# Optimization experiments

Hardware: AMD Instinct MI355X
Metric: run time of the kernel (lower is better)

## Reference

```python
import jax, jax.numpy as jnp
import numpy as np

B, SQ, SKV, E, H = 4, 2048, 2048, 1024, 16
HD = E // H  # 64


def stablemax(x):
    # StableMax: s(x) = x+1 if x>=0 else 1/(1-x), normalized along last axis
    s = jnp.where(x >= 0, x + 1.0, 1.0 / (1.0 - x))
    return s / jnp.sum(s, axis=-1, keepdims=True)


def setup_inputs() -> dict:
    key = jax.random.key(0)
    ks = jax.random.split(key, 6)
    scale = 1.0 / np.sqrt(E)
    return {
        "query": jax.random.normal(ks[0], (B, SQ, E), jnp.float32),
        "key_value": jax.random.normal(ks[1], (B, SKV, E), jnp.float32),
        "Wq": jax.random.normal(ks[2], (E, E), jnp.float32) * scale,
        "bq": jnp.zeros((E,), jnp.float32),
        "Wk": jax.random.normal(ks[3], (E, E), jnp.float32) * scale,
        "bk": jnp.zeros((E,), jnp.float32),
        "Wv": jax.random.normal(ks[4], (E, E), jnp.float32) * scale,
        "bv": jnp.zeros((E,), jnp.float32),
        "Wo": jax.random.normal(ks[5], (E, E), jnp.float32) * scale,
        "bo": jnp.zeros((E,), jnp.float32),
    }


def reference(query, key_value, Wq, bq, Wk, bk, Wv, bv, Wo, bo):
    b = query.shape[0]
    # linear projections (torch Linear: x @ W^T + b)
    q = query @ Wq.T + bq
    k = key_value @ Wk.T + bk
    v = key_value @ Wv.T + bv
    # [B, H, S, HD]
    q = q.reshape(b, -1, H, HD).transpose(0, 2, 1, 3)
    k = k.reshape(b, -1, H, HD).transpose(0, 2, 1, 3)
    v = v.reshape(b, -1, H, HD).transpose(0, 2, 1, 3)
    scores = jnp.einsum("bhqd,bhkd->bhqk", q, k) / np.sqrt(HD).astype(np.float32)
    attn = stablemax(scores)  # dropout is identity in eval mode
    context = jnp.einsum("bhqk,bhkd->bhqd", attn, v)
    context = context.transpose(0, 2, 1, 3).reshape(b, -1, E)
    return context @ Wo.T + bo
```

## Files before the change

### kernel.cpp

```cpp
#include <hip/hip_runtime.h>

typedef __bf16 bf16;
typedef __bf16 bf16x8 __attribute__((ext_vector_type(8)));
typedef __bf16 bf16x4 __attribute__((ext_vector_type(4)));
typedef _Float16 f16;
typedef _Float16 f16x2 __attribute__((ext_vector_type(2)));
typedef _Float16 f16x4 __attribute__((ext_vector_type(4)));
typedef _Float16 f16x8 __attribute__((ext_vector_type(8)));
typedef __fp16 h16x2 __attribute__((ext_vector_type(2)));
typedef float f32x4 __attribute__((ext_vector_type(4)));

__device__ __forceinline__ f32x4 mfma_qk(bf16x8 a, bf16x8 b, f32x4 c) {
    return __builtin_amdgcn_mfma_f32_16x16x32_bf16(a, b, c, 0, 0, 0);
}
__device__ __forceinline__ f32x4 mfma_pv32(f16x8 a, f16x8 b, f32x4 c) {
    return __builtin_amdgcn_mfma_f32_16x16x32_f16(a, b, c, 0, 0, 0);
}
__device__ __forceinline__ f16x2 pkrtz(float a, float b) {
    h16x2 r = __builtin_amdgcn_cvt_pkrtz(a, b);
    return __builtin_bit_cast(f16x2, r);
}

#define GLOAD_LDS16(gp, lp)                                                    \
    __builtin_amdgcn_global_load_lds(                                          \
        (const __attribute__((address_space(1))) unsigned int*)(gp),           \
        (__attribute__((address_space(3))) unsigned int*)(lp), 16, 0, 0)

#define PWAIT4 asm volatile("s_waitcnt vmcnt(4) lgkmcnt(0)\ns_barrier" ::: "memory")
#define PWAIT2 asm volatile("s_waitcnt vmcnt(2) lgkmcnt(0)\ns_barrier" ::: "memory")
#define PWAIT0 asm volatile("s_waitcnt vmcnt(0) lgkmcnt(0)\ns_barrier" ::: "memory")

__global__ __launch_bounds__(256) void cast_inputs(
    const float* __restrict__ w0, const float* __restrict__ w1,
    const float* __restrict__ w2, const float* __restrict__ w3,
    const float* __restrict__ kv, const float* __restrict__ q,
    bf16* __restrict__ Wb, bf16* __restrict__ KVa, bf16* __restrict__ Qb) {
    long i4 = (long)blockIdx.x * 256 + threadIdx.x;
    const float* src;
    bf16* dst;
    long loc;
    float sc = 1.0f;
    if (i4 < 1048576) {
        int which = (int)(i4 >> 18);
        loc = (i4 & 262143) << 2;
        src = which == 0 ? w0 : which == 1 ? w1 : which == 2 ? w2 : w3;
        dst = Wb + ((long)which << 20);
        if (which == 0) sc = 0.125f;
    } else if (i4 < 3145728) {
        loc = (i4 - 1048576) << 2;
        src = kv; dst = KVa;
    } else {
        loc = (i4 - 3145728) << 2;
        src = q; dst = Qb;
    }
    float4 f = *(const float4*)(src + loc);
    bf16x4 o;
    o[0] = (bf16)(f.x * sc); o[1] = (bf16)(f.y * sc);
    o[2] = (bf16)(f.z * sc); o[3] = (bf16)(f.w * sc);
    *(bf16x4*)(dst + loc) = o;
}

__device__ __forceinline__ void gemm_core(
    const bf16* __restrict__ A, const bf16* __restrict__ Wt,
    const float* __restrict__ bias, void* __restrict__ Yv,
    const int om, bf16* smem, const int n0, const int m0, const float bsc) {
    constexpr int Kd = 1024, Nd = 1024;
    constexpr int TP = 132;
    char* sbytes = (char*)smem;
    const int tid = threadIdx.x;
    const int wid = tid >> 6, lane = tid & 63;
    const int l16 = lane & 15, quad = lane >> 4;
    const int mh = (wid >> 1) * 64, nh = (wid & 1) * 64;

    const int rS = tid >> 2;
    const int cS = (tid & 3) ^ (rS & 3);
    const bf16* Asrc = A + (long)(m0 + rS) * Kd + cS * 8;
    const bf16* Bsrc = Wt + (long)(n0 + rS) * Kd + cS * 8;

    const int aOff = (mh + l16) * 64 + ((quad ^ (l16 & 3)) << 4);
    const int bOff = 8192 + (nh + l16) * 64 + ((quad ^ (l16 & 3)) << 4);

    f32x4 acc[4][4];
#pragma unroll
    for (int i = 0; i < 4; ++i)
#pragma unroll
        for (int j = 0; j < 4; ++j) acc[i][j] = (f32x4){0.f, 0.f, 0.f, 0.f};

    auto stageK = [&](int step, int b) {
        const int kt = step * 32;
        char* base = sbytes + b * 16384;
        GLOAD_LDS16(Asrc + kt, base + tid * 16);
        GLOAD_LDS16(Asrc + 64 * Kd + kt, base + 4096 + tid * 16);
        GLOAD_LDS16(Bsrc + kt, base + 8192 + tid * 16);
        GLOAD_LDS16(Bsrc + 64 * Kd + kt, base + 12288 + tid * 16);
    };

    auto computeK = [&](int b) {
        const char* base = sbytes + b * 16384;
        bf16x8 af[4], bq[4];
#pragma unroll
        for (int i = 0; i < 4; ++i) af[i] = *(const bf16x8*)(base + aOff + i * 1024);
#pragma unroll
        for (int i = 0; i < 4; ++i) bq[i] = *(const bf16x8*)(base + bOff + i * 1024);
#pragma unroll
        for (int i = 0; i < 4; ++i)
#pragma unroll
            for (int j = 0; j < 4; ++j)
                acc[i][j] = mfma_qk(af[i], bq[j], acc[i][j]);
    };

    stageK(0, 0);
    stageK(1, 1);
#pragma unroll 1
    for (int t = 0; t < 30; t += 3) {
        PWAIT4; stageK(t + 2, 2); computeK(0);
        PWAIT4; stageK(t + 3, 0); computeK(1);
        PWAIT4; stageK(t + 4, 1); computeK(2);
    }
    PWAIT4; computeK(0);
    PWAIT0; computeK(1);
    __syncthreads();

    if (om == 2) {
#pragma unroll
        for (int j = 0; j < 4; ++j) {
            const int col = nh + j * 16 + l16;
            const float bv = bias[n0 + col] * bsc;
#pragma unroll
            for (int i = 0; i < 4; ++i)
#pragma unroll
                for (int p = 0; p < 2; ++p) {
                    f16x2 pk2;
                    pk2[0] = (f16)(acc[i][j][p * 2 + 0] + bv);
                    pk2[1] = (f16)(acc[i][j][p * 2 + 1] + bv);
                    *(f16x2*)&smem[col * TP + mh + i * 16 + quad * 4 + p * 2] = pk2;
                }
        }
        __syncthreads();
        const int b_ = m0 >> 11, skv0 = m0 & 2047;
        const int rowc = tid & 15;
        const int B32 = (rowc >> 2) * 32, g4 = (rowc & 3) * 4;
        const f16* sm = (const f16*)smem;
#pragma unroll
        for (int c = 0; c < 8; ++c) {
            const int col = (tid >> 4) + c * 16;
            const int colg = n0 + col;
            f16x4 lo = *(const f16x4*)&sm[col * TP + B32 + g4];
            f16x4 hi = *(const f16x4*)&sm[col * TP + B32 + 16 + g4];
            f16x8 v = __builtin_shufflevector(lo, hi, 0, 1, 2, 3, 4, 5, 6, 7);
            const long base = ((long)((b_ * 16 + (colg >> 6)) * 64 + (colg & 63))) << 11;
            *(f16x8*)((f16*)Yv + base + skv0 + rowc * 8) = v;
        }
    } else {
#pragma unroll
        for (int j = 0; j < 4; ++j) {
            const int col = n0 + nh + j * 16 + l16;
            const float bv = bias[col] * bsc;
#pragma unroll
            for (int i = 0; i < 4; ++i)
#pragma unroll
                for (int r = 0; r < 4; ++r) {
                    int row = m0 + mh + i * 16 + quad * 4 + r;
                    float v = acc[i][j][r] + bv;
                    if (om == 1)
                        ((float*)Yv)[(long)row * Nd + col] = v;
                    else
                        ((bf16*)Yv)[(long)row * Nd + col] = (bf16)v;
                }
        }
    }
}

__global__ __launch_bounds__(256) void proj_qkv(
    const bf16* __restrict__ Qb, const bf16* __restrict__ KVa,
    const bf16* __restrict__ Wb,
    const float* __restrict__ bq, const float* __restrict__ bk,
    const float* __restrict__ bv,
    bf16* __restrict__ Qw, bf16* __restrict__ Kw, f16* __restrict__ Vt) {
    __shared__ __align__(16) bf16 smem[24576];
    const int lin = blockIdx.x + (blockIdx.y << 3) + (blockIdx.z << 9);
    const int nid = (lin & 7) * 192 + (lin >> 3);
    const int z = nid >> 9, rem = nid & 511;
    const int n0 = (rem & 7) << 7, m0 = (rem >> 3) << 7;
    if (z == 0)
        gemm_core(Qb, Wb, bq, Qw, 0, smem, n0, m0, 0.125f);
    else if (z == 1)
        gemm_core(KVa, Wb + (1l << 20), bk, Kw, 0, smem, n0, m0, 1.0f);
    else
        gemm_core(KVa, Wb + (2l << 20), bv, Vt, 2, smem, n0, m0, 1.0f);
}

__global__ __launch_bounds__(256) void gemm_o(
    const bf16* __restrict__ Cw, const bf16* __restrict__ Wo,
    const float* __restrict__ bo, float* __restrict__ out) {
    __shared__ __align__(16) bf16 smem[24576];
    const int lin = blockIdx.x + (blockIdx.y << 3);
    const int nid = (lin & 7) * 64 + (lin >> 3);
    gemm_core(Cw, Wo, bo, out, 1, smem, (nid & 7) << 7, (nid >> 3) << 7, 1.0f);
}

__global__ __launch_bounds__(256) void attn_kernel(
    const bf16* __restrict__ Q, const bf16* __restrict__ K,
    const f16* __restrict__ Vt, bf16* __restrict__ C) {
    constexpr int E = 1024, S = 2048;
    __shared__ __align__(16) char smem_raw[24576];

    const int tid = threadIdx.x;
    const int wid = tid >> 6, lane = tid & 63;
    const int l16 = lane & 15, quad = lane >> 4;
    const int l7 = l16 & 7, l3 = l16 & 3;
    const int lin = blockIdx.x + (blockIdx.y << 4) + (blockIdx.z << 8);
    const int nid = (lin & 7) * 128 + (lin >> 3);
    const int qt = nid & 15, h = (nid >> 4) & 15, b = nid >> 8;

    const long q0 = (long)b * S + qt * 128;
    const bf16* Qg = Q + q0 * E + h * 64;
    const bf16* Kg = K + (long)b * S * E + h * 64;
    const f16* Vg = Vt + ((long)(b * 16 + h) << 17);

    bf16x8 qf[2][2];
#pragma unroll
    for (int mt = 0; mt < 2; ++mt)
#pragma unroll
        for (int kc = 0; kc < 2; ++kc)
            qf[mt][kc] = *(const bf16x8*)(Qg + (long)(wid * 32 + mt * 16 + l16) * E + kc * 32 + quad * 8);
    asm volatile("s_waitcnt vmcnt(0)" ::: "memory");

    const bf16* Ksrc = Kg + (long)(tid >> 3) * E + (((tid & 7) ^ ((tid >> 3) & 7)) * 8);
    const f16* Vsrc = Vg + (long)(tid >> 2) * S + (((tid & 3) ^ ((tid >> 2) & 3)) * 8);

    int ka0[3], ka1[3], va[3];
#pragma unroll
    for (int i = 0; i < 3; ++i) {
        ka0[i] = i * 8192 + l16 * 128 + ((quad ^ l7) << 4);
        ka1[i] = i * 8192 + l16 * 128 + (((quad + 4) ^ l7) << 4);
        va[i]  = i * 8192 + 4096 + l16 * 64 + ((quad ^ l3) << 4);
    }

    f16x8 ones8;
#pragma unroll
    for (int j = 0; j < 8; ++j) ones8[j] = (f16)1.0f;

    f32x4 ctx[2][4];
    f32x4 dacc[2];
#pragma unroll
    for (int mt = 0; mt < 2; ++mt) {
        dacc[mt] = (f32x4){0.f, 0.f, 0.f, 0.f};
#pragma unroll
        for (int dt = 0; dt < 4; ++dt) ctx[mt][dt] = (f32x4){0.f, 0.f, 0.f, 0.f};
    }

    auto stage = [&](int kv0, int bi) {
        GLOAD_LDS16(Ksrc + (long)kv0 * E, smem_raw + bi * 8192 + tid * 16);
        GLOAD_LDS16(Vsrc + kv0, smem_raw + bi * 8192 + 4096 + tid * 16);
    };

    auto compute = [&](int bi) {
        f32x4 sacc[2][2];
#pragma unroll
        for (int sh = 0; sh < 2; ++sh) {
            bf16x8 kf0 = *(const bf16x8*)(smem_raw + ka0[bi] + sh * 2048);
            bf16x8 kf1 = *(const bf16x8*)(smem_raw + ka1[bi] + sh * 2048);
            __builtin_amdgcn_s_setprio(1);
#pragma unroll
            for (int mt = 0; mt < 2; ++mt) {
                f32x4 t = mfma_qk(kf0, qf[mt][0], (f32x4){0.f, 0.f, 0.f, 0.f});
                sacc[sh][mt] = mfma_qk(kf1, qf[mt][1], t);
            }
            __builtin_amdgcn_s_setprio(0);
        }
        f16x8 pp[2];
#pragma unroll
        for (int mt = 0; mt < 2; ++mt) {
            float sv[8];
#pragma unroll
            for (int sh = 0; sh < 2; ++sh)
#pragma unroll
                for (int r = 0; r < 4; ++r) {
                    float x = sacc[sh][mt][r];
                    float u = __builtin_fabsf(x) + 1.0f;
                    sv[sh * 4 + r] = (x >= 0.f) ? u : __builtin_amdgcn_rcpf(u);
                }
            f16x2 w0 = pkrtz(sv[0], sv[1]);
            f16x2 w1 = pkrtz(sv[2], sv[3]);
            f16x2 w2 = pkrtz(sv[4], sv[5]);
            f16x2 w3 = pkrtz(sv[6], sv[7]);
            f16x4 lo = __builtin_shufflevector(w0, w1, 0, 1, 2, 3);
            f16x4 hi = __builtin_shufflevector(w2, w3, 0, 1, 2, 3);
            pp[mt] = __builtin_shufflevector(lo, hi, 0, 1, 2, 3, 4, 5, 6, 7);
        }
        __builtin_amdgcn_s_setprio(1);
        dacc[0] = mfma_pv32(ones8, pp[0], dacc[0]);
        dacc[1] = mfma_pv32(ones8, pp[1], dacc[1]);
        __builtin_amdgcn_s_setprio(0);
#pragma unroll
        for (int dt = 0; dt < 4; ++dt) {
            f16x8 vf = *(const f16x8*)(smem_raw + va[bi] + dt * 1024);
            __builtin_amdgcn_s_setprio(1);
#pragma unroll
            for (int mt = 0; mt < 2; ++mt)
                ctx[mt][dt] = mfma_pv32(vf, pp[mt], ctx[mt][dt]);
            __builtin_amdgcn_s_setprio(0);
        }
    };

    stage(0, 0);
    stage(32, 1);
    int kv = 64;
#pragma unroll 1
    for (int it = 0; it < 20; ++it) {
        PWAIT2; stage(kv, 2); compute(0); kv += 32;
        PWAIT2; stage(kv, 0); compute(1); kv += 32;
        PWAIT2; stage(kv, 1); compute(2); kv += 32;
    }
    PWAIT2; stage(kv, 2); compute(0);
    PWAIT2; stage(kv + 32, 0); compute(1);
    PWAIT2; compute(2);
    PWAIT0; compute(0);
    __syncthreads();

    float scl[2];
#pragma unroll
    for (int mt = 0; mt < 2; ++mt) scl[mt] = __builtin_amdgcn_rcpf(dacc[mt][0]);

    bf16* Os = (bf16*)smem_raw;
#pragma unroll
    for (int mt = 0; mt < 2; ++mt)
#pragma unroll
        for (int dt = 0; dt < 4; ++dt) {
            bf16x4 o;
#pragma unroll
            for (int r = 0; r < 4; ++r) o[r] = (bf16)(ctx[mt][dt][r] * scl[mt]);
            *(bf16x4*)&Os[(wid * 32 + mt * 16 + l16) * 68 + dt * 16 + quad * 4] = o;
        }
    __syncthreads();
    {
        const int r = tid >> 1, c = (tid & 1) * 32;
        bf16* cp = C + (q0 + r) * E + h * 64 + c;
#pragma unroll
        for (int j = 0; j < 4; ++j)
            *(bf16x8*)(cp + j * 8) = *(const bf16x8*)&Os[r * 68 + c + j * 8];
    }
}

extern "C" void kernel_launch(void* const* d_in, const int* in_sizes, int n_in,
                              void* d_out, int out_size, void* d_ws, size_t ws_size,
                              hipStream_t stream) {
    const float* query = (const float*)d_in[0];
    const float* keyv  = (const float*)d_in[1];
    const float* Wq = (const float*)d_in[2];
    const float* bq = (const float*)d_in[3];
    const float* Wk = (const float*)d_in[4];
    const float* bk = (const float*)d_in[5];
    const float* Wv = (const float*)d_in[6];
    const float* bv = (const float*)d_in[7];
    const float* Wo = (const float*)d_in[8];
    const float* bo = (const float*)d_in[9];

    char* ws = (char*)d_ws;
    bf16* Wb  = (bf16*)ws;
    bf16* KVa = (bf16*)(ws + (8l << 20));
    bf16* Qb  = (bf16*)(ws + (24l << 20));
    bf16* Qw  = (bf16*)(ws + (40l << 20));
    f16*  Vt  = (f16*)(ws + (56l << 20));
    bf16* Kw  = (bf16*)d_out;
    bf16* Cw  = KVa;

    cast_inputs<<<20480, 256, 0, stream>>>(Wq, Wk, Wv, Wo, keyv, query, Wb, KVa, Qb);

    proj_qkv<<<dim3(8, 64, 3), 256, 0, stream>>>(Qb, KVa, Wb, bq, bk, bv, Qw, Kw, Vt);

    attn_kernel<<<dim3(16, 16, 4), 256, 0, stream>>>(Qw, Kw, Vt, Cw);

    gemm_o<<<dim3(8, 64), 256, 0, stream>>>(Cw, Wb + (3l << 20), bo, (float*)d_out);
}
```

Before: 309.6 us.

## Rewrite output GEMM with 128x64 tiles and triple-buffered pipeline; grid-stride cast

Replaces the shared gemm_core call for the output projection with a dedicated kernel using 128x64 tiles, a K step of 32 and a three-stage global-to-LDS ring buffer with vmcnt(3) waits. The grid doubles to 1024 blocks, which should fill the GPU's compute units better for the 8192x1024 output GEMM. The cast kernel becomes a grid-stride loop over a quarter as many blocks, so each thread converts several elements. Smaller tiles lower per-block reuse and add more A-tile reloads.

```diff
diff --git a/kernel.cpp b/kernel.cpp
--- a/kernel.cpp
+++ b/kernel.cpp
@@ -27,6 +27,7 @@
         (__attribute__((address_space(3))) unsigned int*)(lp), 16, 0, 0)
 
 #define PWAIT4 asm volatile("s_waitcnt vmcnt(4) lgkmcnt(0)\ns_barrier" ::: "memory")
+#define PWAIT3 asm volatile("s_waitcnt vmcnt(3) lgkmcnt(0)\ns_barrier" ::: "memory")
 #define PWAIT2 asm volatile("s_waitcnt vmcnt(2) lgkmcnt(0)\ns_barrier" ::: "memory")
 #define PWAIT0 asm volatile("s_waitcnt vmcnt(0) lgkmcnt(0)\ns_barrier" ::: "memory")
 
@@ -35,29 +36,31 @@
     const float* __restrict__ w2, const float* __restrict__ w3,
     const float* __restrict__ kv, const float* __restrict__ q,
     bf16* __restrict__ Wb, bf16* __restrict__ KVa, bf16* __restrict__ Qb) {
-    long i4 = (long)blockIdx.x * 256 + threadIdx.x;
-    const float* src;
-    bf16* dst;
-    long loc;
-    float sc = 1.0f;
-    if (i4 < 1048576) {
-        int which = (int)(i4 >> 18);
-        loc = (i4 & 262143) << 2;
-        src = which == 0 ? w0 : which == 1 ? w1 : which == 2 ? w2 : w3;
-        dst = Wb + ((long)which << 20);
-        if (which == 0) sc = 0.125f;
-    } else if (i4 < 3145728) {
-        loc = (i4 - 1048576) << 2;
-        src = kv; dst = KVa;
-    } else {
-        loc = (i4 - 3145728) << 2;
-        src = q; dst = Qb;
-    }
-    float4 f = *(const float4*)(src + loc);
-    bf16x4 o;
-    o[0] = (bf16)(f.x * sc); o[1] = (bf16)(f.y * sc);
-    o[2] = (bf16)(f.z * sc); o[3] = (bf16)(f.w * sc);
-    *(bf16x4*)(dst + loc) = o;
+    for (long i4 = (long)blockIdx.x * 256 + threadIdx.x; i4 < 5242880;
+         i4 += 5120l * 256) {
+        const float* src;
+        bf16* dst;
+        long loc;
+        float sc = 1.0f;
+        if (i4 < 1048576) {
+            int which = (int)(i4 >> 18);
+            loc = (i4 & 262143) << 2;
+            src = which == 0 ? w0 : which == 1 ? w1 : which == 2 ? w2 : w3;
+            dst = Wb + ((long)which << 20);
+            if (which == 0) sc = 0.125f;
+        } else if (i4 < 3145728) {
+            loc = (i4 - 1048576) << 2;
+            src = kv; dst = KVa;
+        } else {
+            loc = (i4 - 3145728) << 2;
+            src = q; dst = Qb;
+        }
+        float4 f = *(const float4*)(src + loc);
+        bf16x4 o;
+        o[0] = (bf16)(f.x * sc); o[1] = (bf16)(f.y * sc);
+        o[2] = (bf16)(f.z * sc); o[3] = (bf16)(f.w * sc);
+        *(bf16x4*)(dst + loc) = o;
+    }
 }
 
 __device__ __forceinline__ void gemm_core(
@@ -193,10 +196,75 @@
 __global__ __launch_bounds__(256) void gemm_o(
     const bf16* __restrict__ Cw, const bf16* __restrict__ Wo,
     const float* __restrict__ bo, float* __restrict__ out) {
-    __shared__ __align__(16) bf16 smem[24576];
-    const int lin = blockIdx.x + (blockIdx.y << 3);
-    const int nid = (lin & 7) * 64 + (lin >> 3);
-    gemm_core(Cw, Wo, bo, out, 1, smem, (nid & 7) << 7, (nid >> 3) << 7, 1.0f);
+    constexpr int Kd = 1024, Nd = 1024;
+    __shared__ __align__(16) char sb[36864];
+    const int tid = threadIdx.x;
+    const int wid = tid >> 6, lane = tid & 63;
+    const int l16 = lane & 15, quad = lane >> 4;
+    const int lin = blockIdx.x + (blockIdx.y << 4);
+    const int nid = (lin & 7) * 128 + (lin >> 3);
+    const int n0 = (nid & 15) << 6, m0 = (nid >> 4) << 7;
+    const int mh = (wid >> 1) * 64, nh = (wid & 1) * 32;
+
+    const int rS = tid >> 2;
+    const int cS = (tid & 3) ^ (rS & 3);
+    const bf16* Asrc = Cw + (long)(m0 + rS) * Kd + cS * 8;
+    const bf16* Bsrc = Wo + (long)(n0 + rS) * Kd + cS * 8;
+
+    const int aOff = (mh + l16) * 64 + ((quad ^ (l16 & 3)) << 4);
+    const int bOff = 8192 + (nh + l16) * 64 + ((quad ^ (l16 & 3)) << 4);
+
+    f32x4 acc[4][2];
+#pragma unroll
+    for (int i = 0; i < 4; ++i)
+#pragma unroll
+        for (int j = 0; j < 2; ++j) acc[i][j] = (f32x4){0.f, 0.f, 0.f, 0.f};
+
+    auto stageK = [&](int step, int b) {
+        const int kt = step * 32;
+        char* base = sb + b * 12288;
+        GLOAD_LDS16(Asrc + kt, base + tid * 16);
+        GLOAD_LDS16(Asrc + 64 * Kd + kt, base + 4096 + tid * 16);
+        GLOAD_LDS16(Bsrc + kt, base + 8192 + tid * 16);
+    };
+
+    auto computeK = [&](int b) {
+        const char* base = sb + b * 12288;
+        bf16x8 af[4], bq[2];
+#pragma unroll
+        for (int i = 0; i < 4; ++i) af[i] = *(const bf16x8*)(base + aOff + i * 1024);
+#pragma unroll
+        for (int i = 0; i < 2; ++i) bq[i] = *(const bf16x8*)(base + bOff + i * 1024);
+#pragma unroll
+        for (int i = 0; i < 4; ++i)
+#pragma unroll
+            for (int j = 0; j < 2; ++j)
+                acc[i][j] = mfma_qk(af[i], bq[j], acc[i][j]);
+    };
+
+    stageK(0, 0);
+    stageK(1, 1);
+#pragma unroll 1
+    for (int t = 0; t < 30; t += 3) {
+        PWAIT3; stageK(t + 2, 2); computeK(0);
+        PWAIT3; stageK(t + 3, 0); computeK(1);
+        PWAIT3; stageK(t + 4, 1); computeK(2);
+    }
+    PWAIT3; computeK(0);
+    PWAIT0; computeK(1);
+
+#pragma unroll
+    for (int j = 0; j < 2; ++j) {
+        const int col = n0 + nh + j * 16 + l16;
+        const float bv = bo[col];
+#pragma unroll
+        for (int i = 0; i < 4; ++i)
+#pragma unroll
+            for (int r = 0; r < 4; ++r) {
+                int row = m0 + mh + i * 16 + quad * 4 + r;
+                out[(long)row * Nd + col] = acc[i][j][r] + bv;
+            }
+    }
 }
 
 __global__ __launch_bounds__(256) void attn_kernel(
@@ -366,11 +434,11 @@
     bf16* Kw  = (bf16*)d_out;
     bf16* Cw  = KVa;
 
-    cast_inputs<<<20480, 256, 0, stream>>>(Wq, Wk, Wv, Wo, keyv, query, Wb, KVa, Qb);
+    cast_inputs<<<5120, 256, 0, stream>>>(Wq, Wk, Wv, Wo, keyv, query, Wb, KVa, Qb);
 
     proj_qkv<<<dim3(8, 64, 3), 256, 0, stream>>>(Qb, KVa, Wb, bq, bk, bv, Qw, Kw, Vt);
 
     attn_kernel<<<dim3(16, 16, 4), 256, 0, stream>>>(Qw, Kw, Vt, Cw);
 
-    gemm_o<<<dim3(8, 64), 256, 0, stream>>>(Cw, Wb + (3l << 20), bo, (float*)d_out);
-}
+    gemm_o<<<dim3(16, 64), 256, 0, stream>>>(Cw, Wb + (3l << 20), bo, (float*)d_out);
+}
```

After: 318.3 us. +2.8%, slower.
